# Optimization experiments

Measured on AMD Instinct MI355X. Metric: run time of the kernel, lower is better.

Reference implementation:

```python
import jax, jax.numpy as jnp
import numpy as np

TOP_K = 4


def setup_inputs() -> dict:
    key = jax.random.key(0)
    k1, k2, k3 = jax.random.split(key, 3)
    T, H, E = 16384, 2880, 128
    hidden_states = jax.random.normal(k1, (T, H), dtype=jnp.float32)
    weight = jax.random.normal(k2, (E, H), dtype=jnp.float32) * 0.02
    bias = jax.random.normal(k3, (E,), dtype=jnp.float32) * 0.02
    return {"hidden_states": hidden_states, "weight": weight, "bias": bias}


def reference(hidden_states, weight, bias):
    # [T, H] @ [H, E] + [E] -> router logits [T, E]
    hidden_states = hidden_states.reshape(-1, weight.shape[1])
    router_logits = jnp.einsum('th,eh->te', hidden_states, weight) + bias
    # top-k over experts, then softmax over the k selected logits
    router_top_value, router_indices = jax.lax.top_k(router_logits, TOP_K)
    router_scores = jax.nn.softmax(router_top_value, axis=-1)
    return router_scores, router_indices
```

## Files before the change

kernel.cpp:

```cpp
#include <hip/hip_runtime.h>
#include <math.h>

#define T_TOKENS 16384
#define H_DIM    2880
#define E_EXP    128
#define TOPK     4
#define MT       32
#define KC       32
#define EPS_GAP  5e-4f

typedef __bf16 bf16x8 __attribute__((ext_vector_type(8)));
typedef float  f32x4  __attribute__((ext_vector_type(4)));

__device__ __forceinline__ unsigned short bf16_rn(float x) {
    unsigned int u = __float_as_uint(x);
    unsigned int r = (u + 0x7fffu + ((u >> 16) & 1u)) >> 16;
    return (unsigned short)r;
}
__device__ __forceinline__ float bf16_tof(unsigned short h) {
    return __uint_as_float(((unsigned int)h) << 16);
}
__device__ __forceinline__ unsigned int pack2(unsigned short a, unsigned short b) {
    return (unsigned int)a | ((unsigned int)b << 16);
}

__global__ __launch_bounds__(256, 2) void router_main(
    const float* __restrict__ A, const float* __restrict__ W,
    const float* __restrict__ bias, float* __restrict__ out,
    int* __restrict__ flag_count, int* __restrict__ flag_list)
{
    __shared__ __align__(16) uint2 sAhi[2][128];
    __shared__ __align__(16) uint2 sAlo[2][128];
    __shared__ __align__(16) uint4 sWhi[8][64];
    __shared__ __align__(16) uint4 sWlo[8][64];
    __shared__ float sL[MT][129];

    const int tid    = threadIdx.x;
    const int t_base = blockIdx.x * MT;

    const int wave = tid >> 6;
    const int L    = tid & 63;
    const int wm   = wave & 1;
    const int wn   = wave >> 1;

    const int at = tid >> 3;
    const int ac = tid & 7;
    const int a_idx = (at >> 4) * 128 + ((((ac >> 1) << 4) | (at & 15)) << 1) + (ac & 1);
    const float* Ag = A + (size_t)(t_base + at) * H_DIM + ac * 4;
    const int we  = tid >> 1;
    const int wq0 = (tid & 1) * 2;
    const float* Wg = W + (size_t)we * H_DIM + wq0 * 8;
    const int w_nt = we >> 4;
    const int w_n  = we & 15;

    f32x4 acc[4];
#pragma unroll
    for (int i = 0; i < 4; ++i) { f32x4 z = {0.f, 0.f, 0.f, 0.f}; acc[i] = z; }

    uint2* sAhiF = &sAhi[0][0];
    uint2* sAloF = &sAlo[0][0];

    for (int k0 = 0; k0 < H_DIM; k0 += KC) {
        const float4 av  = *(const float4*)(Ag + k0);
        const float4 wv0 = *(const float4*)(Wg + k0);
        const float4 wv1 = *(const float4*)(Wg + k0 + 4);
        const float4 wv2 = *(const float4*)(Wg + k0 + 8);
        const float4 wv3 = *(const float4*)(Wg + k0 + 12);

        float af[4] = {av.x, av.y, av.z, av.w};
        unsigned short ah[4], al[4];
#pragma unroll
        for (int j = 0; j < 4; ++j) {
            ah[j] = bf16_rn(af[j]);
            al[j] = bf16_rn(af[j] - bf16_tof(ah[j]));
        }
        const uint2 ahp = make_uint2(pack2(ah[0], ah[1]), pack2(ah[2], ah[3]));
        const uint2 alp = make_uint2(pack2(al[0], al[1]), pack2(al[2], al[3]));

        float wf[16] = {wv0.x, wv0.y, wv0.z, wv0.w, wv1.x, wv1.y, wv1.z, wv1.w,
                        wv2.x, wv2.y, wv2.z, wv2.w, wv3.x, wv3.y, wv3.z, wv3.w};
        unsigned short wh[16], wl[16];
#pragma unroll
        for (int j = 0; j < 16; ++j) {
            wh[j] = bf16_rn(wf[j]);
            wl[j] = bf16_rn(wf[j] - bf16_tof(wh[j]));
        }
        const uint4 whp0 = make_uint4(pack2(wh[0], wh[1]), pack2(wh[2], wh[3]),
                                      pack2(wh[4], wh[5]), pack2(wh[6], wh[7]));
        const uint4 whp1 = make_uint4(pack2(wh[8], wh[9]), pack2(wh[10], wh[11]),
                                      pack2(wh[12], wh[13]), pack2(wh[14], wh[15]));
        const uint4 wlp0 = make_uint4(pack2(wl[0], wl[1]), pack2(wl[2], wl[3]),
                                      pack2(wl[4], wl[5]), pack2(wl[6], wl[7]));
        const uint4 wlp1 = make_uint4(pack2(wl[8], wl[9]), pack2(wl[10], wl[11]),
                                      pack2(wl[12], wl[13]), pack2(wl[14], wl[15]));

        __syncthreads();

        sAhiF[a_idx] = ahp;
        sAloF[a_idx] = alp;
        sWhi[w_nt][((wq0 + 0) << 4) | w_n] = whp0;
        sWhi[w_nt][((wq0 + 1) << 4) | w_n] = whp1;
        sWlo[w_nt][((wq0 + 0) << 4) | w_n] = wlp0;
        sWlo[w_nt][((wq0 + 1) << 4) | w_n] = wlp1;

        __syncthreads();

        const bf16x8 ahi = *(const bf16x8*)&sAhi[wm][L * 2];
        const bf16x8 alo = *(const bf16x8*)&sAlo[wm][L * 2];
#pragma unroll
        for (int i = 0; i < 4; ++i) {
            const int nt = wn * 4 + i;
            const bf16x8 whi = *(const bf16x8*)&sWhi[nt][L];
            const bf16x8 wlo = *(const bf16x8*)&sWlo[nt][L];
            acc[i] = __builtin_amdgcn_mfma_f32_16x16x32_bf16(ahi, whi, acc[i], 0, 0, 0);
            acc[i] = __builtin_amdgcn_mfma_f32_16x16x32_bf16(ahi, wlo, acc[i], 0, 0, 0);
            acc[i] = __builtin_amdgcn_mfma_f32_16x16x32_bf16(alo, whi, acc[i], 0, 0, 0);
        }
    }

#pragma unroll
    for (int i = 0; i < 4; ++i) {
        const int e = wn * 64 + i * 16 + (L & 15);
        const float b = bias[e];
#pragma unroll
        for (int r = 0; r < 4; ++r) {
            const int tl = wm * 16 + (L >> 4) * 4 + r;
            sL[tl][e] = acc[i][r] + b;
        }
    }
    __syncthreads();

    if (tid < MT) {
        float v0 = -1e30f, v1 = -1e30f, v2 = -1e30f, v3 = -1e30f, v4 = -1e30f;
        int   i0 = 0, i1 = 0, i2 = 0, i3 = 0, i4 = 0;
        for (int e = 0; e < E_EXP; ++e) {
            const float x = sL[tid][e];
            if (x > v4) {
                if (x > v0)      { v4=v3;i4=i3; v3=v2;i3=i2; v2=v1;i2=i1; v1=v0;i1=i0; v0=x;i0=e; }
                else if (x > v1) { v4=v3;i4=i3; v3=v2;i3=i2; v2=v1;i2=i1; v1=x;i1=e; }
                else if (x > v2) { v4=v3;i4=i3; v3=v2;i3=i2; v2=x;i2=e; }
                else if (x > v3) { v4=v3;i4=i3; v3=x;i3=e; }
                else             { v4=x;i4=e; }
            }
        }
        const float g0 = v0 - v1, g1 = v1 - v2, g2 = v2 - v3, g3 = v3 - v4;
        float mg = g0 < g1 ? g0 : g1;
        mg = mg < g2 ? mg : g2;
        mg = mg < g3 ? mg : g3;

        const float e0x = expf(v0 - v0);
        const float e1x = expf(v1 - v0);
        const float e2x = expf(v2 - v0);
        const float e3x = expf(v3 - v0);
        const float s   = e0x + e1x + e2x + e3x;

        const int gt = t_base + tid;
        float* out_scores = out;
        float* out_idx    = out + (size_t)T_TOKENS * TOPK;
        out_scores[gt * 4 + 0] = e0x / s;
        out_scores[gt * 4 + 1] = e1x / s;
        out_scores[gt * 4 + 2] = e2x / s;
        out_scores[gt * 4 + 3] = e3x / s;
        out_idx[gt * 4 + 0] = (float)i0;
        out_idx[gt * 4 + 1] = (float)i1;
        out_idx[gt * 4 + 2] = (float)i2;
        out_idx[gt * 4 + 3] = (float)i3;

        if (mg < EPS_GAP) {
            const int p = atomicAdd(flag_count, 1);
            if (p < T_TOKENS) flag_list[p] = gt;
        }
    }
}

__global__ __launch_bounds__(256) void router_recheck(
    const float* __restrict__ A, const float* __restrict__ W,
    const float* __restrict__ bias, float* __restrict__ out,
    const int* __restrict__ flag_count, const int* __restrict__ flag_list)
{
    __shared__ double sPart[256];
    __shared__ double sLog[E_EXP];

    int count = *flag_count;
    if (count > T_TOKENS) count = T_TOKENS;

    const int tid = threadIdx.x;
    const int e   = tid & (E_EXP - 1);
    const int h   = tid >> 7;

    for (int i = blockIdx.x; i < count; i += gridDim.x) {
        const int t = flag_list[i];
        const float* arow = A + (size_t)t * H_DIM;
        const float* wrow = W + (size_t)e * H_DIM;
        const int k0 = h * (H_DIM / 2);

        double s0 = 0.0, s1 = 0.0, s2 = 0.0, s3 = 0.0;
        for (int k = k0; k < k0 + H_DIM / 2; k += 4) {
            s0 += (double)arow[k + 0] * (double)wrow[k + 0];
            s1 += (double)arow[k + 1] * (double)wrow[k + 1];
            s2 += (double)arow[k + 2] * (double)wrow[k + 2];
            s3 += (double)arow[k + 3] * (double)wrow[k + 3];
        }
        sPart[tid] = (s0 + s1) + (s2 + s3);
        __syncthreads();
        if (h == 0) sLog[e] = sPart[e] + sPart[e + 128] + (double)bias[e];
        __syncthreads();

        if (tid == 0) {
            double v0 = -1e300, v1 = -1e300, v2 = -1e300, v3 = -1e300;
            int    i0 = 0, i1 = 0, i2 = 0, i3 = 0;
            for (int q = 0; q < E_EXP; ++q) {
                const double x = sLog[q];
                if (x > v3) {
                    if (x > v0)      { v3=v2;i3=i2; v2=v1;i2=i1; v1=v0;i1=i0; v0=x;i0=q; }
                    else if (x > v1) { v3=v2;i3=i2; v2=v1;i2=i1; v1=x;i1=q; }
                    else if (x > v2) { v3=v2;i3=i2; v2=x;i2=q; }
                    else             { v3=x;i3=q; }
                }
            }
            const double e0x = exp(v0 - v0);
            const double e1x = exp(v1 - v0);
            const double e2x = exp(v2 - v0);
            const double e3x = exp(v3 - v0);
            const double s   = e0x + e1x + e2x + e3x;
            float* out_scores = out;
            float* out_idx    = out + (size_t)T_TOKENS * TOPK;
            out_scores[t * 4 + 0] = (float)(e0x / s);
            out_scores[t * 4 + 1] = (float)(e1x / s);
            out_scores[t * 4 + 2] = (float)(e2x / s);
            out_scores[t * 4 + 3] = (float)(e3x / s);
            out_idx[t * 4 + 0] = (float)i0;
            out_idx[t * 4 + 1] = (float)i1;
            out_idx[t * 4 + 2] = (float)i2;
            out_idx[t * 4 + 3] = (float)i3;
        }
        __syncthreads();
    }
}

extern "C" void kernel_launch(void* const* d_in, const int* in_sizes, int n_in,
                              void* d_out, int out_size, void* d_ws, size_t ws_size,
                              hipStream_t stream) {
    const float* A    = (const float*)d_in[0];
    const float* W    = (const float*)d_in[1];
    const float* bias = (const float*)d_in[2];
    float* out = (float*)d_out;

    int* flag_count = (int*)d_ws;
    int* flag_list  = (int*)d_ws + 1;

    hipMemsetAsync(flag_count, 0, sizeof(int), stream);
    router_main<<<dim3(T_TOKENS / MT), dim3(256), 0, stream>>>(A, W, bias, out,
                                                               flag_count, flag_list);
    router_recheck<<<dim3(256), dim3(256), 0, stream>>>(A, W, bias, out,
                                                        flag_count, flag_list);
}
```

Before: 419.2 us.

## Split K across two wave groups in router GEMM and vectorize conversions

Doubles the block to 512 threads and splits the hidden dimension into two halves, each processed by its own group of four waves with separate shared buffers. The partial logits are then combined in shared memory. The manual bf16 hi/lo split is replaced with packed __float22bfloat162_rn conversions, and the fp64 recheck loop uses float4 loads. The aim is more latency hiding and fewer conversion instructions, at the cost of more shared memory per block and an extra reduction step.

```diff
diff --git a/kernel.cpp b/kernel.cpp
--- a/kernel.cpp
+++ b/kernel.cpp
@@ -1,8 +1,10 @@
 #include <hip/hip_runtime.h>
+#include <hip/hip_bf16.h>
 #include <math.h>
 
 #define T_TOKENS 16384
 #define H_DIM    2880
+#define KHALF    1440
 #define E_EXP    128
 #define TOPK     4
 #define MT       32
@@ -12,120 +14,122 @@
 typedef __bf16 bf16x8 __attribute__((ext_vector_type(8)));
 typedef float  f32x4  __attribute__((ext_vector_type(4)));
 
-__device__ __forceinline__ unsigned short bf16_rn(float x) {
-    unsigned int u = __float_as_uint(x);
-    unsigned int r = (u + 0x7fffu + ((u >> 16) & 1u)) >> 16;
-    return (unsigned short)r;
-}
-__device__ __forceinline__ float bf16_tof(unsigned short h) {
-    return __uint_as_float(((unsigned int)h) << 16);
-}
-__device__ __forceinline__ unsigned int pack2(unsigned short a, unsigned short b) {
-    return (unsigned int)a | ((unsigned int)b << 16);
-}
-
-__global__ __launch_bounds__(256, 2) void router_main(
+__device__ __forceinline__ void split2(float a, float b,
+                                       unsigned int& hi, unsigned int& lo) {
+    float2 p; p.x = a; p.y = b;
+    __hip_bfloat162 h = __float22bfloat162_rn(p);
+    unsigned int hu; __builtin_memcpy(&hu, &h, 4);
+    float2 r;
+    r.x = a - __uint_as_float((hu & 0xffffu) << 16);
+    r.y = b - __uint_as_float(hu & 0xffff0000u);
+    __hip_bfloat162 l = __float22bfloat162_rn(r);
+    unsigned int lu; __builtin_memcpy(&lu, &l, 4);
+    hi = hu; lo = lu;
+}
+
+__global__ __launch_bounds__(512, 4) void router_main(
     const float* __restrict__ A, const float* __restrict__ W,
     const float* __restrict__ bias, float* __restrict__ out,
     int* __restrict__ flag_count, int* __restrict__ flag_list)
 {
-    __shared__ __align__(16) uint2 sAhi[2][128];
-    __shared__ __align__(16) uint2 sAlo[2][128];
-    __shared__ __align__(16) uint4 sWhi[8][64];
-    __shared__ __align__(16) uint4 sWlo[8][64];
+    __shared__ __align__(16) uint2 sAhi[2][2][128];
+    __shared__ __align__(16) uint2 sAlo[2][2][128];
+    __shared__ __align__(16) uint4 sWhi[2][8][64];
+    __shared__ __align__(16) uint4 sWlo[2][8][64];
     __shared__ float sL[MT][129];
 
     const int tid    = threadIdx.x;
     const int t_base = blockIdx.x * MT;
 
-    const int wave = tid >> 6;
-    const int L    = tid & 63;
-    const int wm   = wave & 1;
-    const int wn   = wave >> 1;
-
-    const int at = tid >> 3;
-    const int ac = tid & 7;
+    const int wave  = tid >> 6;
+    const int L     = tid & 63;
+    const int whalf = wave >> 2;
+    const int wm    = wave & 1;
+    const int wn    = (wave >> 1) & 1;
+
+    const int shalf = tid >> 8;
+    const int tid_h = tid & 255;
+    const int at = tid_h >> 3;
+    const int ac = tid_h & 7;
     const int a_idx = (at >> 4) * 128 + ((((ac >> 1) << 4) | (at & 15)) << 1) + (ac & 1);
-    const float* Ag = A + (size_t)(t_base + at) * H_DIM + ac * 4;
-    const int we  = tid >> 1;
-    const int wq0 = (tid & 1) * 2;
-    const float* Wg = W + (size_t)we * H_DIM + wq0 * 8;
+    const float* Ag = A + (size_t)(t_base + at) * H_DIM + shalf * KHALF + ac * 4;
+    const int we  = tid_h >> 1;
+    const int wq0 = (tid_h & 1) * 2;
+    const float* Wg = W + (size_t)we * H_DIM + shalf * KHALF + wq0 * 8;
     const int w_nt = we >> 4;
     const int w_n  = we & 15;
 
+    uint2* sAhiF = &sAhi[shalf][0][0];
+    uint2* sAloF = &sAlo[shalf][0][0];
+
     f32x4 acc[4];
 #pragma unroll
     for (int i = 0; i < 4; ++i) { f32x4 z = {0.f, 0.f, 0.f, 0.f}; acc[i] = z; }
 
-    uint2* sAhiF = &sAhi[0][0];
-    uint2* sAloF = &sAlo[0][0];
-
-    for (int k0 = 0; k0 < H_DIM; k0 += KC) {
+    for (int k0 = 0; k0 < KHALF; k0 += KC) {
         const float4 av  = *(const float4*)(Ag + k0);
         const float4 wv0 = *(const float4*)(Wg + k0);
         const float4 wv1 = *(const float4*)(Wg + k0 + 4);
         const float4 wv2 = *(const float4*)(Wg + k0 + 8);
         const float4 wv3 = *(const float4*)(Wg + k0 + 12);
 
-        float af[4] = {av.x, av.y, av.z, av.w};
-        unsigned short ah[4], al[4];
-#pragma unroll
-        for (int j = 0; j < 4; ++j) {
-            ah[j] = bf16_rn(af[j]);
-            al[j] = bf16_rn(af[j] - bf16_tof(ah[j]));
-        }
-        const uint2 ahp = make_uint2(pack2(ah[0], ah[1]), pack2(ah[2], ah[3]));
-        const uint2 alp = make_uint2(pack2(al[0], al[1]), pack2(al[2], al[3]));
-
-        float wf[16] = {wv0.x, wv0.y, wv0.z, wv0.w, wv1.x, wv1.y, wv1.z, wv1.w,
-                        wv2.x, wv2.y, wv2.z, wv2.w, wv3.x, wv3.y, wv3.z, wv3.w};
-        unsigned short wh[16], wl[16];
-#pragma unroll
-        for (int j = 0; j < 16; ++j) {
-            wh[j] = bf16_rn(wf[j]);
-            wl[j] = bf16_rn(wf[j] - bf16_tof(wh[j]));
-        }
-        const uint4 whp0 = make_uint4(pack2(wh[0], wh[1]), pack2(wh[2], wh[3]),
-                                      pack2(wh[4], wh[5]), pack2(wh[6], wh[7]));
-        const uint4 whp1 = make_uint4(pack2(wh[8], wh[9]), pack2(wh[10], wh[11]),
-                                      pack2(wh[12], wh[13]), pack2(wh[14], wh[15]));
-        const uint4 wlp0 = make_uint4(pack2(wl[0], wl[1]), pack2(wl[2], wl[3]),
-                                      pack2(wl[4], wl[5]), pack2(wl[6], wl[7]));
-        const uint4 wlp1 = make_uint4(pack2(wl[8], wl[9]), pack2(wl[10], wl[11]),
-                                      pack2(wl[12], wl[13]), pack2(wl[14], wl[15]));
+        uint2 ahp, alp;
+        split2(av.x, av.y, ahp.x, alp.x);
+        split2(av.z, av.w, ahp.y, alp.y);
+
+        uint4 whp0, wlp0, whp1, wlp1;
+        split2(wv0.x, wv0.y, whp0.x, wlp0.x);
+        split2(wv0.z, wv0.w, whp0.y, wlp0.y);
+        split2(wv1.x, wv1.y, whp0.z, wlp0.z);
+        split2(wv1.z, wv1.w, whp0.w, wlp0.w);
+        split2(wv2.x, wv2.y, whp1.x, wlp1.x);
+        split2(wv2.z, wv2.w, whp1.y, wlp1.y);
+        split2(wv3.x, wv3.y, whp1.z, wlp1.z);
+        split2(wv3.z, wv3.w, whp1.w, wlp1.w);
 
         __syncthreads();
 
         sAhiF[a_idx] = ahp;
         sAloF[a_idx] = alp;
-        sWhi[w_nt][((wq0 + 0) << 4) | w_n] = whp0;
-        sWhi[w_nt][((wq0 + 1) << 4) | w_n] = whp1;
-        sWlo[w_nt][((wq0 + 0) << 4) | w_n] = wlp0;
-        sWlo[w_nt][((wq0 + 1) << 4) | w_n] = wlp1;
-
-        __syncthreads();
-
-        const bf16x8 ahi = *(const bf16x8*)&sAhi[wm][L * 2];
-        const bf16x8 alo = *(const bf16x8*)&sAlo[wm][L * 2];
+        sWhi[shalf][w_nt][((wq0 + 0) << 4) | w_n] = whp0;
+        sWhi[shalf][w_nt][((wq0 + 1) << 4) | w_n] = whp1;
+        sWlo[shalf][w_nt][((wq0 + 0) << 4) | w_n] = wlp0;
+        sWlo[shalf][w_nt][((wq0 + 1) << 4) | w_n] = wlp1;
+
+        __syncthreads();
+
+        const bf16x8 ahi = *(const bf16x8*)&sAhi[whalf][wm][L * 2];
+        const bf16x8 alo = *(const bf16x8*)&sAlo[whalf][wm][L * 2];
 #pragma unroll
         for (int i = 0; i < 4; ++i) {
             const int nt = wn * 4 + i;
-            const bf16x8 whi = *(const bf16x8*)&sWhi[nt][L];
-            const bf16x8 wlo = *(const bf16x8*)&sWlo[nt][L];
+            const bf16x8 whi = *(const bf16x8*)&sWhi[whalf][nt][L];
+            const bf16x8 wlo = *(const bf16x8*)&sWlo[whalf][nt][L];
             acc[i] = __builtin_amdgcn_mfma_f32_16x16x32_bf16(ahi, whi, acc[i], 0, 0, 0);
             acc[i] = __builtin_amdgcn_mfma_f32_16x16x32_bf16(ahi, wlo, acc[i], 0, 0, 0);
             acc[i] = __builtin_amdgcn_mfma_f32_16x16x32_bf16(alo, whi, acc[i], 0, 0, 0);
         }
     }
 
-#pragma unroll
-    for (int i = 0; i < 4; ++i) {
-        const int e = wn * 64 + i * 16 + (L & 15);
-        const float b = bias[e];
-#pragma unroll
-        for (int r = 0; r < 4; ++r) {
-            const int tl = wm * 16 + (L >> 4) * 4 + r;
-            sL[tl][e] = acc[i][r] + b;
+    __syncthreads();
+    if (whalf == 0) {
+#pragma unroll
+        for (int i = 0; i < 4; ++i) {
+            const int e = wn * 64 + i * 16 + (L & 15);
+            const float b = bias[e];
+#pragma unroll
+            for (int r = 0; r < 4; ++r)
+                sL[wm * 16 + (L >> 4) * 4 + r][e] = acc[i][r] + b;
+        }
+    }
+    __syncthreads();
+    if (whalf == 1) {
+#pragma unroll
+        for (int i = 0; i < 4; ++i) {
+            const int e = wn * 64 + i * 16 + (L & 15);
+#pragma unroll
+            for (int r = 0; r < 4; ++r)
+                sL[wm * 16 + (L >> 4) * 4 + r][e] += acc[i][r];
         }
     }
     __syncthreads();
@@ -195,11 +199,19 @@
         const int k0 = h * (H_DIM / 2);
 
         double s0 = 0.0, s1 = 0.0, s2 = 0.0, s3 = 0.0;
-        for (int k = k0; k < k0 + H_DIM / 2; k += 4) {
-            s0 += (double)arow[k + 0] * (double)wrow[k + 0];
-            s1 += (double)arow[k + 1] * (double)wrow[k + 1];
-            s2 += (double)arow[k + 2] * (double)wrow[k + 2];
-            s3 += (double)arow[k + 3] * (double)wrow[k + 3];
+        for (int k = k0; k < k0 + H_DIM / 2; k += 8) {
+            const float4 a0 = *(const float4*)(arow + k);
+            const float4 a1 = *(const float4*)(arow + k + 4);
+            const float4 w0 = *(const float4*)(wrow + k);
+            const float4 w1 = *(const float4*)(wrow + k + 4);
+            s0 += (double)a0.x * (double)w0.x;
+            s1 += (double)a0.y * (double)w0.y;
+            s2 += (double)a0.z * (double)w0.z;
+            s3 += (double)a0.w * (double)w0.w;
+            s0 += (double)a1.x * (double)w1.x;
+            s1 += (double)a1.y * (double)w1.y;
+            s2 += (double)a1.z * (double)w1.z;
+            s3 += (double)a1.w * (double)w1.w;
         }
         sPart[tid] = (s0 + s1) + (s2 + s3);
         __syncthreads();
@@ -250,7 +262,7 @@
     int* flag_list  = (int*)d_ws + 1;
 
     hipMemsetAsync(flag_count, 0, sizeof(int), stream);
-    router_main<<<dim3(T_TOKENS / MT), dim3(256), 0, stream>>>(A, W, bias, out,
+    router_main<<<dim3(T_TOKENS / MT), dim3(512), 0, stream>>>(A, W, bias, out,
                                                                flag_count, flag_list);
     router_recheck<<<dim3(256), dim3(256), 0, stream>>>(A, W, bias, out,
                                                         flag_count, flag_list);
```

Result: faster. 392.0 us (-6.5%).
